# Performance work log

Hardware: AMD Instinct MI355X
Metric: run time of the kernel (lower is better)

## Reference

```python
import math
import jax, jax.numpy as jnp
import numpy as np

STEP = 0.1
EPS = 1e-12


def _laplacian(src, dst, n):
    # dense symmetric-normalized Laplacian from COO edge list (symmetrized, 0/1 weights)
    A = jnp.zeros((n, n), dtype=jnp.float32).at[src, dst].set(1.0)
    A = jnp.maximum(A, A.T)
    deg = A.sum(axis=1)
    dinv = jnp.where(deg > 0, 1.0 / jnp.sqrt(jnp.maximum(deg, 1e-12)), 0.0)
    return jnp.eye(n, dtype=jnp.float32) - dinv[:, None] * A * dinv[None, :]


def _filter_bank(L, bs):
    # rational band-pass bank centered at b in arange(0,2.1,STEP):
    # D_b = sqrt(2)*a * inv((L - b I)^4 + a I),  a = (STEP/2)^4
    n = L.shape[0]
    a = (STEP / 2.0) ** 4
    I = jnp.eye(n, dtype=L.dtype)

    def one(b):
        M1 = L - b * I
        P2 = M1 @ M1
        P4 = P2 @ P2
        return math.sqrt(2.0) * a * jnp.linalg.inv(P4 + a * I)

    return jax.vmap(one)(bs)  # [F, n, n]


def _cdist_mean(e):
    # mean pairwise euclidean distance, safe sqrt on the zero diagonal
    d2 = jnp.sum((e[:, None, :] - e[None, :, :]) ** 2, axis=-1)
    d = jnp.sqrt(jnp.where(d2 > 0, d2, 1.0))
    return jnp.where(d2 > 0, d, 0.0).mean()


def setup_inputs() -> dict:
    key = jax.random.key(0)
    k1, k2, k3, k4, k5 = jax.random.split(key, 5)
    B, N, F0, R, E = 64, 128, 32, 1118, 512
    return {
        "x": jax.random.normal(k1, (B, N, F0), dtype=jnp.float32),
        "random_signal": jax.random.normal(k2, (B, N, R), dtype=jnp.float32),
        "C": jax.random.normal(k3, (21, 1), dtype=jnp.float32),
        "edge_src": jax.random.randint(k4, (B, E), 0, N),
        "edge_dst": jax.random.randint(k5, (B, E), 0, N),
        "num_classes": 4,
    }


def reference(x, random_signal, C, edge_src, edge_dst, num_classes):
    B, N, _ = x.shape
    R = random_signal.shape[-1]
    # torch.normal(0, sqrt(1/R)) random signal concatenated to features
    feats = jnp.concatenate([x, random_signal * math.sqrt(1.0 / R)], axis=-1)  # [B,N,F0+R]
    bs = jnp.arange(0.0, 2.1, STEP, dtype=jnp.float32)  # [21]
    Cn = C / jnp.maximum(jnp.linalg.norm(C, axis=0, keepdims=True), EPS)  # F.normalize(C, dim=0)

    def per_graph(src, dst, xg):
        L = _laplacian(src, dst, N)
        D = _filter_bank(L, bs)                      # [F,N,N]
        L_hat = jnp.einsum('fnm,f->nm', D, Cn[:, 0])  # D.permute(1,2,0) @ C, squeezed
        A_hat = jnp.eye(N, dtype=xg.dtype) - L_hat
        y = A_hat @ xg                                # [N, F0+R]
        z = y / jnp.maximum(jnp.linalg.norm(y, axis=1, keepdims=True), EPS)
        logits = z @ z.T                              # decode_all on normalized x
        sp = -jnp.abs(logits).sum() / (N * N)         # -||logits||_1 / n^2
        return y.mean(axis=0), sp

    emb, sp_terms = jax.vmap(per_graph)(edge_src, edge_dst, feats)  # [B,D], [B]

    # faithful repeated in-loop division: s_{i+1} = (s_i + t_i)/B  =>  sum_i t_i * B^{-(B-i)}
    i = jnp.arange(B, dtype=jnp.float32)
    w = jnp.exp(-(B - i) * jnp.log(float(B)))
    sparsity_fwd = jnp.sum(sp_terms * w)

    # labels y = arange(B) % num_classes; one positive group (class members) and
    # one negative group (non-members) per class
    idx = np.arange(B)
    hl1 = jnp.float32(0.0)
    hl2 = jnp.float32(0.0)
    for c in range(num_classes):
        pos = jnp.asarray(idx[idx % num_classes == c])
        neg = jnp.asarray(idx[idx % num_classes != c])
        beta = 1.0 / num_classes + 1e-13  # one group per class
        hl1 = hl1 + (-_cdist_mean(emb[neg])) / beta
        hl2 = hl2 + _cdist_mean(emb[pos])

    Fk = C.shape[0]
    dims = jnp.sqrt(jnp.float32(Fk))
    c_l1 = jnp.sum(jnp.abs(C), axis=0)
    c_l2 = jnp.maximum(jnp.linalg.norm(C, axis=0), EPS)
    sparsity_c = jnp.mean((dims - c_l1 / c_l2) / (dims - 1.0))

    return sparsity_c + hl2 + hl1 + sparsity_fwd
```

## Files before the change

### kernel.cpp

```cpp
#include <hip/hip_runtime.h>
#include <math.h>

#define NN 128
#define SM 129
#define TS 132
#define RS 132
#define SS 17
#define SD 130
#define EP 132

typedef double d4 __attribute__((ext_vector_type(4)));

__global__ __launch_bounds__(256) void k1_lap(
    const int* __restrict__ src, const int* __restrict__ dst,
    int E, float* __restrict__ Lout) {
  extern __shared__ float sm1[];
  float* A    = sm1;
  float* dinv = sm1 + NN * SM;
  const int g   = blockIdx.x;
  const int tid = threadIdx.x;

  for (int e = tid; e < NN * NN; e += 256) {
    int i = e >> 7, j = e & 127;
    A[i * SM + j] = 0.f;
  }
  __syncthreads();
  const int* s = src + (size_t)g * E;
  const int* d = dst + (size_t)g * E;
  for (int e = tid; e < E; e += 256) {
    int a = s[e], b = d[e];
    A[a * SM + b] = 1.f;
    A[b * SM + a] = 1.f;
  }
  __syncthreads();
  if (tid < NN) {
    float acc = 0.f;
    for (int j = 0; j < NN; ++j) acc += A[tid * SM + j];
    dinv[tid] = (acc > 0.f) ? (float)(1.0 / sqrt((double)acc)) : 0.f;
  }
  __syncthreads();
  float* Lg = Lout + (size_t)g * NN * NN;
  for (int e = tid; e < NN * NN; e += 256) {
    int i = e >> 7, j = e & 127;
    Lg[e] = ((i == j) ? 1.f : 0.f) - dinv[i] * dinv[j] * A[i * SM + j];
  }
}

__global__ __launch_bounds__(512, 1) void kpow2(
    const float* __restrict__ L, double* __restrict__ L2) {
  extern __shared__ double Bs[];
  const int bid = blockIdx.x;
  const int g = bid >> 2, q = bid & 3;
  const int tid = threadIdx.x;
  const int wv = tid >> 6, ln = tid & 63;
  const int m  = ln & 15, kq = ln >> 4;
  const int rb = 32 * q + 16 * (wv & 1);
  const int cb0 = 2 * (wv >> 1);

  int rIdx[4], cIdx[4];
  {
    d4 z = {0.0, 0.0, 0.0, 0.0};
    d4 pr = __builtin_amdgcn_mfma_f64_16x16x4f64((double)m, 1.0, z, 0, 0, 0);
    d4 pc = __builtin_amdgcn_mfma_f64_16x16x4f64(1.0, (double)m, z, 0, 0, 0);
#pragma unroll
    for (int r = 0; r < 4; ++r) {
      rIdx[r] = ((int)(pr[r] * 0.25 + 0.5)) & 15;
      cIdx[r] = ((int)(pc[r] * 0.25 + 0.5)) & 15;
    }
  }

  const float* Lg = L + (size_t)g * NN * NN;
  for (int e = tid; e < NN * NN; e += 512) {
    int i = e >> 7, j = e & 127;
    Bs[i * SD + j] = (double)Lg[e];
  }
  __syncthreads();

  d4 acc[2];
#pragma unroll
  for (int c = 0; c < 2; ++c) {
    acc[c][0] = 0.0; acc[c][1] = 0.0; acc[c][2] = 0.0; acc[c][3] = 0.0;
  }
  for (int kc = 0; kc < 32; ++kc) {
    double a = Bs[(rb + m) * SD + 4 * kc + kq];
#pragma unroll
    for (int c = 0; c < 2; ++c) {
      double b = Bs[(4 * kc + kq) * SD + 16 * (cb0 + c) + m];
      acc[c] = __builtin_amdgcn_mfma_f64_16x16x4f64(a, b, acc[c], 0, 0, 0);
    }
  }
  double* out = L2 + (size_t)g * NN * NN;
#pragma unroll
  for (int c = 0; c < 2; ++c)
#pragma unroll
    for (int r = 0; r < 4; ++r)
      out[(rb + rIdx[r]) * NN + 16 * (cb0 + c) + cIdx[r]] = acc[c][r];
}

__global__ __launch_bounds__(512, 1) void kpow34(
    const float* __restrict__ L, const double* __restrict__ L2,
    double* __restrict__ L3, double* __restrict__ L4) {
  extern __shared__ double Bs[];
  const int bid = blockIdx.x;
  const int g = bid >> 2, h = (bid >> 1) & 1, job = bid & 1;
  const int tid = threadIdx.x;
  const int wv = tid >> 6, ln = tid & 63;
  const int m  = ln & 15, kq = ln >> 4;
  const int rb = 64 * h + 16 * (wv & 3);
  const int cb0 = 4 * (wv >> 2);

  int rIdx[4], cIdx[4];
  {
    d4 z = {0.0, 0.0, 0.0, 0.0};
    d4 pr = __builtin_amdgcn_mfma_f64_16x16x4f64((double)m, 1.0, z, 0, 0, 0);
    d4 pc = __builtin_amdgcn_mfma_f64_16x16x4f64(1.0, (double)m, z, 0, 0, 0);
#pragma unroll
    for (int r = 0; r < 4; ++r) {
      rIdx[r] = ((int)(pr[r] * 0.25 + 0.5)) & 15;
      cIdx[r] = ((int)(pc[r] * 0.25 + 0.5)) & 15;
    }
  }

  const float*  Lg  = L  + (size_t)g * NN * NN;
  const double* L2g = L2 + (size_t)g * NN * NN;
  if (job == 0) {
    for (int e = tid; e < NN * NN; e += 512) {
      int i = e >> 7, j = e & 127;
      Bs[i * SD + j] = (double)Lg[e];
    }
  } else {
    for (int e = tid; e < NN * NN; e += 512) {
      int i = e >> 7, j = e & 127;
      Bs[i * SD + j] = L2g[e];
    }
  }
  __syncthreads();

  d4 acc[4];
#pragma unroll
  for (int c = 0; c < 4; ++c) {
    acc[c][0] = 0.0; acc[c][1] = 0.0; acc[c][2] = 0.0; acc[c][3] = 0.0;
  }
  for (int kc = 0; kc < 32; ++kc) {
    double a = L2g[(rb + m) * NN + 4 * kc + kq];
#pragma unroll
    for (int c = 0; c < 4; ++c) {
      double b = Bs[(4 * kc + kq) * SD + 16 * (cb0 + c) + m];
      acc[c] = __builtin_amdgcn_mfma_f64_16x16x4f64(a, b, acc[c], 0, 0, 0);
    }
  }
  double* out = (job == 0 ? L3 : L4) + (size_t)g * NN * NN;
#pragma unroll
  for (int c = 0; c < 4; ++c)
#pragma unroll
    for (int r = 0; r < 4; ++r)
      out[(rb + rIdx[r]) * NN + 16 * (cb0 + c) + cIdx[r]] = acc[c][r];
}

__global__ __launch_bounds__(512, 4) void k2_filter(
    const float* __restrict__ L, const double* __restrict__ L2,
    const double* __restrict__ L3, const double* __restrict__ L4,
    const float* __restrict__ C, int NF, float* __restrict__ W) {
  extern __shared__ char smraw[];
  double* Rp  = (double*)smraw;
  double* Scd = (double*)(smraw + 16 * RS * 8);
  double* Pv  = (double*)(smraw + 16 * RS * 8 + 8 * 16 * SS * 8);

  const int bid = blockIdx.x;
  const int g = bid / NF, f = bid % NF;
  const int tid = threadIdx.x;
  const int wv = tid >> 6, ln = tid & 63;
  const int m  = ln & 15, kq = ln >> 4;
  double* S = Scd + wv * 16 * SS;

  double csum = 0.0;
  for (int q = 0; q < NF; ++q) { double c = (double)C[q]; csum += c * c; }
  double cn = sqrt(csum); if (cn < 1e-12) cn = 1e-12;
  const double a4 = 6.25e-6;
  const double coef = 1.4142135623730951 * a4 * ((double)C[f] / cn);
  const float  bf = (float)((double)f * 0.1);
  const double bb = (double)bf;
  const double c3 = -4.0 * bb;
  const double c2 = 6.0 * bb * bb;
  const double c1 = -4.0 * bb * bb * bb;
  const double c0 = bb * bb * bb * bb + a4;

  int rIdx[4], cIdx[4];
  {
    d4 z = {0.0, 0.0, 0.0, 0.0};
    d4 pr = __builtin_amdgcn_mfma_f64_16x16x4f64((double)m, 1.0, z, 0, 0, 0);
    d4 pc = __builtin_amdgcn_mfma_f64_16x16x4f64(1.0, (double)m, z, 0, 0, 0);
#pragma unroll
    for (int r = 0; r < 4; ++r) {
      rIdx[r] = ((int)(pr[r] * 0.25 + 0.5)) & 15;
      cIdx[r] = ((int)(pc[r] * 0.25 + 0.5)) & 15;
    }
  }

  const float*  Lg  = L  + (size_t)g * NN * NN;
  const double* L2g = L2 + (size_t)g * NN * NN;
  const double* L3g = L3 + (size_t)g * NN * NN;
  const double* L4g = L4 + (size_t)g * NN * NN;
  d4 T[8];
#pragma unroll
  for (int cb = 0; cb < 8; ++cb)
#pragma unroll
    for (int r = 0; r < 4; ++r) {
      int i = 16 * wv + rIdx[r], j = 16 * cb + cIdx[r];
      int idx = i * NN + j;
      double v = L4g[idx];
      v = fma(c3, L3g[idx], v);
      v = fma(c2, L2g[idx], v);
      v = fma(c1, (double)Lg[idx], v);
      if (i == j) v += c0;
      T[cb][r] = v;
    }

#pragma unroll 1
  for (int t = 0; t < 8; ++t) {
    if (wv == t) {
#pragma unroll
      for (int cb = 0; cb < 8; ++cb)
#pragma unroll
        for (int r = 0; r < 4; ++r)
          Rp[rIdx[r] * RS + 16 * cb + cIdx[r]] = T[cb][r];
    }
    __syncthreads();

    if (wv == t) {
      double sr[4];
#pragma unroll
      for (int r = 0; r < 4; ++r) sr[r] = Rp[(4 * r + kq) * RS + 16 * t + m];
#pragma unroll
      for (int k = 0; k < 16; ++k) {
        const int kr = k >> 2, kl = k & 3;
        double pv   = __shfl(sr[kr], 16 * kl + k);
        double rowv = __shfl(sr[kr], 16 * kl + m);
        double cv[4];
#pragma unroll
        for (int r = 0; r < 4; ++r) cv[r] = __shfl(sr[r], 16 * kq + k);
        double dp = 1.0 / pv;
#pragma unroll
        for (int r = 0; r < 4; ++r) {
          int i = 4 * r + kq;
          double nv;
          if (i == k)      nv = (m == k) ? dp : rowv * dp;
          else if (m == k) nv = -cv[r] * dp;
          else             nv = fma(-(cv[r] * dp), rowv, sr[r]);
          sr[r] = nv;
        }
      }
#pragma unroll
      for (int r = 0; r < 4; ++r) Pv[(4 * r + kq) * SS + m] = sr[r];
    }
    __syncthreads();

#pragma unroll
    for (int cb = 0; cb < 8; ++cb) {
      if (cb != t) continue;
      if (wv == t) {
#pragma unroll
        for (int r = 0; r < 4; ++r) T[cb][r] = Pv[rIdx[r] * SS + cIdx[r]];
      } else {
#pragma unroll
        for (int r = 0; r < 4; ++r) S[rIdx[r] * SS + cIdx[r]] = T[cb][r];
        __builtin_amdgcn_wave_barrier();
        d4 ncv = {0.0, 0.0, 0.0, 0.0};
#pragma unroll
        for (int kc = 0; kc < 4; ++kc) {
          double a = S[m * SS + 4 * kc + kq];
          double b = -Pv[(4 * kc + kq) * SS + m];
          ncv = __builtin_amdgcn_mfma_f64_16x16x4f64(a, b, ncv, 0, 0, 0);
        }
        T[cb] = ncv;
        __builtin_amdgcn_wave_barrier();
#pragma unroll
        for (int r = 0; r < 4; ++r) S[rIdx[r] * SS + cIdx[r]] = T[cb][r];
      }
    }
    __builtin_amdgcn_wave_barrier();

    const double* asrc = (wv == t) ? Pv : S;
#pragma unroll
    for (int cb = 0; cb < 8; ++cb) {
      if (cb == t) continue;
      d4 acc;
      if (wv == t) { acc[0] = 0.0; acc[1] = 0.0; acc[2] = 0.0; acc[3] = 0.0; }
      else         { acc = T[cb]; }
#pragma unroll
      for (int kc = 0; kc < 4; ++kc) {
        double a = asrc[m * SS + 4 * kc + kq];
        double b = Rp[(4 * kc + kq) * RS + 16 * cb + m];
        acc = __builtin_amdgcn_mfma_f64_16x16x4f64(a, b, acc, 0, 0, 0);
      }
      T[cb] = acc;
    }
    __syncthreads();
  }

  float* Wg = W + (size_t)g * NN * NN;
#pragma unroll
  for (int cb = 0; cb < 8; ++cb)
#pragma unroll
    for (int r = 0; r < 4; ++r)
      atomicAdd(&Wg[(16 * wv + rIdx[r]) * NN + 16 * cb + cIdx[r]],
                (float)(coef * T[cb][r]));
}

__global__ __launch_bounds__(512, 1) void k3_fused(
    const float* __restrict__ x, const float* __restrict__ rs,
    const float* __restrict__ W, float* __restrict__ G,
    float* __restrict__ emb, int F0, int R, int DTOT, int NCH,
    float rscale) {
  extern __shared__ float sm3[];
  float* ldsW = sm3;
  float* ldsX = sm3 + NN * TS;
  const int bid = blockIdx.x;
  const int g = bid / NCH;
  const int c = bid % NCH;
  const int d0 = c * 128;
  const int tid = threadIdx.x, tr = tid >> 4, tc = tid & 15;

  const float* Wg = W + (size_t)g * NN * NN;
  for (int e = tid; e < NN * NN; e += 512) {
    int k = e >> 7, i = e & 127;
    ldsW[k * TS + i] = Wg[e];
  }
  const float* xg = x + (size_t)g * NN * F0;
  const float* rg = rs + (size_t)g * NN * R;
  for (int e = tid; e < NN * NN; e += 512) {
    int k = e >> 7, dl = e & 127;
    int d = d0 + dl;
    float v = 0.f;
    if (d < DTOT) v = (d < F0) ? xg[k * F0 + d] : rg[k * R + (d - F0)] * rscale;
    ldsX[k * TS + dl] = v;
  }
  __syncthreads();

  float acc[4][8];
#pragma unroll
  for (int v = 0; v < 4; ++v)
#pragma unroll
    for (int u = 0; u < 8; ++u) acc[v][u] = 0.f;
  for (int k = 0; k < NN; ++k) {
    float4 w4 = *(const float4*)(ldsW + k * TS + 4 * tr);
    float xv[8];
#pragma unroll
    for (int u = 0; u < 8; ++u) xv[u] = ldsX[k * TS + tc + 16 * u];
    float wvv[4] = {w4.x, w4.y, w4.z, w4.w};
#pragma unroll
    for (int v = 0; v < 4; ++v)
#pragma unroll
      for (int u = 0; u < 8; ++u) acc[v][u] = fmaf(wvv[v], xv[u], acc[v][u]);
  }
#pragma unroll
  for (int v = 0; v < 4; ++v)
#pragma unroll
    for (int u = 0; u < 8; ++u)
      acc[v][u] = ldsX[(4 * tr + v) * TS + tc + 16 * u] - acc[v][u];
  __syncthreads();

#pragma unroll
  for (int v = 0; v < 4; ++v)
#pragma unroll
    for (int u = 0; u < 8; ++u)
      ldsW[(tc + 16 * u) * TS + 4 * tr + v] = acc[v][u];
#pragma unroll
  for (int u = 0; u < 8; ++u) {
    float s = 0.f;
#pragma unroll
    for (int v = 0; v < 4; ++v) s += acc[v][u];
    ldsX[tr * EP + tc + 16 * u] = s;
  }
  __syncthreads();

  float gg[4][8];
#pragma unroll
  for (int v = 0; v < 4; ++v)
#pragma unroll
    for (int u = 0; u < 8; ++u) gg[v][u] = 0.f;
  for (int dl = 0; dl < NN; ++dl) {
    float4 a4v = *(const float4*)(ldsW + dl * TS + 4 * tr);
    float bv[8];
#pragma unroll
    for (int u = 0; u < 8; ++u) bv[u] = ldsW[dl * TS + tc + 16 * u];
    float av[4] = {a4v.x, a4v.y, a4v.z, a4v.w};
#pragma unroll
    for (int v = 0; v < 4; ++v)
#pragma unroll
      for (int u = 0; u < 8; ++u) gg[v][u] = fmaf(av[v], bv[u], gg[v][u]);
  }
  float* Gg = G + (size_t)g * NN * NN;
#pragma unroll
  for (int v = 0; v < 4; ++v)
#pragma unroll
    for (int u = 0; u < 8; ++u)
      atomicAdd(&Gg[(4 * tr + v) * NN + tc + 16 * u], gg[v][u]);

  if (tid < 128) {
    int d = d0 + tid;
    if (d < DTOT) {
      float s = 0.f;
      for (int tt = 0; tt < 32; ++tt) s += ldsX[tt * EP + tid];
      emb[(size_t)g * 1152 + d] = s * (1.f / 128.f);
    }
  }
}

__global__ __launch_bounds__(256) void k45_fused(
    const float* __restrict__ G, double* __restrict__ spt,
    const float* __restrict__ emb, float* __restrict__ Dm, int DTOT) {
  __shared__ float inr[NN];
  __shared__ double red[4];
  const int bid = blockIdx.x, tid = threadIdx.x;
  if (bid < 64) {
    const int g = bid;
    const float* Gg = G + (size_t)g * NN * NN;
    if (tid < NN) {
      float n = sqrtf(fmaxf(Gg[tid * NN + tid], 0.f));
      inr[tid] = 1.f / fmaxf(n, 1e-12f);
    }
    __syncthreads();
    double s = 0.0;
    for (int e = tid; e < NN * NN; e += 256) {
      int i = e >> 7, j = e & 127;
      s += (double)(fabsf(Gg[e]) * inr[i] * inr[j]);
    }
    for (int off = 32; off; off >>= 1) s += __shfl_down(s, off);
    int wave = tid >> 6, lane = tid & 63;
    if (lane == 0) red[wave] = s;
    __syncthreads();
    if (tid == 0) spt[g] = -(red[0] + red[1] + red[2] + red[3]) / (double)(NN * NN);
  } else {
    const int i = bid - 64;
    const int wv = tid >> 6, l = tid & 63;
    float ei[18];
#pragma unroll
    for (int s = 0; s < 18; ++s) {
      int d = l + 64 * s;
      ei[s] = (d < DTOT) ? emb[(size_t)i * 1152 + d] : 0.f;
    }
    for (int jj = 0; jj < 16; ++jj) {
      int j = 4 * jj + wv;
      float acc = 0.f;
#pragma unroll
      for (int s = 0; s < 18; ++s) {
        int d = l + 64 * s;
        if (d < DTOT) {
          float df = ei[s] - emb[(size_t)j * 1152 + d];
          acc = fmaf(df, df, acc);
        }
      }
      for (int off = 32; off; off >>= 1) acc += __shfl_down(acc, off);
      if (l == 0) Dm[i * 64 + j] = (acc > 0.f) ? sqrtf(acc) : 0.f;
    }
  }
}

__global__ __launch_bounds__(64) void k5b_final(
    const float* __restrict__ Dm, const double* __restrict__ spt,
    const float* __restrict__ C, int NF,
    const int* __restrict__ ncls, float* __restrict__ out) {
  const int lane = threadIdx.x;
  const int nc = ncls[0];
  double spf = spt[lane] * exp(-((double)(64 - lane)) * log(64.0));
  for (int off = 32; off; off >>= 1) spf += __shfl_down(spf, off);

  double hl1 = 0.0, hl2 = 0.0;
  const double beta = 1.0 / (double)nc + 1e-13;
  for (int cc = 0; cc < nc; ++cc) {
    bool ip = (lane % nc) == cc;
    double ps = 0.0, ns = 0.0;
    for (int j = 0; j < 64; ++j) {
      double dv = (double)Dm[lane * 64 + j];
      bool jp = (j % nc) == cc;
      if (ip && jp) ps += dv;
      if (!ip && !jp) ns += dv;
    }
    for (int off = 32; off; off >>= 1) {
      ps += __shfl_down(ps, off);
      ns += __shfl_down(ns, off);
    }
    int npos = 0;
    for (int q = 0; q < 64; ++q) if (q % nc == cc) npos++;
    int nneg = 64 - npos;
    hl2 += ps / ((double)npos * (double)npos);
    hl1 += -(ns / ((double)nneg * (double)nneg)) / beta;
  }
  if (lane == 0) {
    double l1 = 0.0, l2 = 0.0;
    for (int q = 0; q < NF; ++q) { double cv = (double)C[q]; l1 += fabs(cv); l2 += cv * cv; }
    l2 = sqrt(l2); if (l2 < 1e-12) l2 = 1e-12;
    double dims = sqrt((double)NF);
    double sc = (dims - l1 / l2) / (dims - 1.0);
    out[0] = (float)(sc + hl2 + hl1 + spf);
  }
}

extern "C" void kernel_launch(void* const* d_in, const int* in_sizes, int n_in,
                              void* d_out, int out_size, void* d_ws, size_t ws_size,
                              hipStream_t stream) {
  (void)n_in; (void)out_size; (void)ws_size;
  const float* x    = (const float*)d_in[0];
  const float* rs   = (const float*)d_in[1];
  const float* C    = (const float*)d_in[2];
  const int*   esrc = (const int*)d_in[3];
  const int*   edst = (const int*)d_in[4];
  const int*   ncls = (const int*)d_in[5];
  float* out = (float*)d_out;

  const int F0   = in_sizes[0] / (64 * 128);
  const int R    = in_sizes[1] / (64 * 128);
  const int NF   = in_sizes[2];
  const int E    = in_sizes[3] / 64;
  const int DTOT = F0 + R;
  const int NCH  = (DTOT + 127) / 128;
  const float rscale = (float)(1.0 / sqrt((double)R));

  char* ws = (char*)d_ws;
  size_t off = 0;
  float*  L    = (float*)(ws + off);  off += (size_t)64 * NN * NN * 4;
  float*  W    = (float*)(ws + off);  off += (size_t)64 * NN * NN * 4;
  float*  G    = (float*)(ws + off);  off += (size_t)64 * NN * NN * 4;
  double* L2d  = (double*)(ws + off); off += (size_t)64 * NN * NN * 8;
  double* L3d  = (double*)(ws + off); off += (size_t)64 * NN * NN * 8;
  double* L4d  = (double*)(ws + off); off += (size_t)64 * NN * NN * 8;
  float*  emb  = (float*)(ws + off);  off += (size_t)64 * 1152 * 4;
  double* spt  = (double*)(ws + off); off += (size_t)64 * 8;
  float*  Dm   = (float*)(ws + off);  off += (size_t)64 * 64 * 4;

  hipMemsetAsync(W, 0, (size_t)2 * 64 * NN * NN * 4, stream);

  const int lds1 = (NN * SM + NN) * 4;
  const int ldsp = NN * SD * 8;
  const int lds2 = 16 * RS * 8 + 8 * 16 * SS * 8 + 16 * SS * 8;
  const int lds3 = NN * TS * 4 * 2;
  hipFuncSetAttribute((const void*)k1_lap,    hipFuncAttributeMaxDynamicSharedMemorySize, lds1);
  hipFuncSetAttribute((const void*)kpow2,     hipFuncAttributeMaxDynamicSharedMemorySize, ldsp);
  hipFuncSetAttribute((const void*)kpow34,    hipFuncAttributeMaxDynamicSharedMemorySize, ldsp);
  hipFuncSetAttribute((const void*)k2_filter, hipFuncAttributeMaxDynamicSharedMemorySize, lds2);
  hipFuncSetAttribute((const void*)k3_fused,  hipFuncAttributeMaxDynamicSharedMemorySize, lds3);

  k1_lap<<<64, 256, lds1, stream>>>(esrc, edst, E, L);
  kpow2<<<256, 512, ldsp, stream>>>(L, L2d);
  kpow34<<<256, 512, ldsp, stream>>>(L, L2d, L3d, L4d);
  k2_filter<<<64 * NF, 512, lds2, stream>>>(L, L2d, L3d, L4d, C, NF, W);
  k3_fused<<<64 * NCH, 512, lds3, stream>>>(x, rs, W, G, emb, F0, R, DTOT, NCH, rscale);
  k45_fused<<<128, 256, 0, stream>>>(G, spt, emb, Dm, DTOT);
  k5b_final<<<1, 64, 0, stream>>>(Dm, spt, C, NF, ncls, out);
}
```

Baseline: 637.1 us.

## Pipeline block Gauss-Jordan pivot inversion with double-buffered row panels

Restructures the blocked Gauss-Jordan inverse in the filter kernel so that, after each step's trailing update, the next pivot wave publishes its row panel and inverts its 16x16 pivot block immediately, writing into double-buffered LDS (Rp0/Rp1, Pv0/Pv1). This removes two of the three __syncthreads per step and lets the serial pivot inversion overlap with other waves' MFMA updates. It costs extra LDS per block, which may reduce occupancy, and adds more intra-wave barriers.

```diff
diff --git a/kernel.cpp b/kernel.cpp
--- a/kernel.cpp
+++ b/kernel.cpp
@@ -157,14 +157,38 @@
       out[(rb + rIdx[r]) * NN + 16 * (cb0 + c) + cIdx[r]] = acc[c][r];
 }
 
+__device__ __forceinline__ void gj16(double sr[4], int m, int kq) {
+#pragma unroll
+  for (int k = 0; k < 16; ++k) {
+    const int kr = k >> 2, kl = k & 3;
+    double pv   = __shfl(sr[kr], 16 * kl + k);
+    double rowv = __shfl(sr[kr], 16 * kl + m);
+    double cv[4];
+#pragma unroll
+    for (int r = 0; r < 4; ++r) cv[r] = __shfl(sr[r], 16 * kq + k);
+    double dp = 1.0 / pv;
+#pragma unroll
+    for (int r = 0; r < 4; ++r) {
+      int i = 4 * r + kq;
+      double nv;
+      if (i == k)      nv = (m == k) ? dp : rowv * dp;
+      else if (m == k) nv = -cv[r] * dp;
+      else             nv = fma(-(cv[r] * dp), rowv, sr[r]);
+      sr[r] = nv;
+    }
+  }
+}
+
 __global__ __launch_bounds__(512, 4) void k2_filter(
     const float* __restrict__ L, const double* __restrict__ L2,
     const double* __restrict__ L3, const double* __restrict__ L4,
     const float* __restrict__ C, int NF, float* __restrict__ W) {
   extern __shared__ char smraw[];
-  double* Rp  = (double*)smraw;
-  double* Scd = (double*)(smraw + 16 * RS * 8);
-  double* Pv  = (double*)(smraw + 16 * RS * 8 + 8 * 16 * SS * 8);
+  double* Rp0 = (double*)smraw;
+  double* Rp1 = Rp0 + 16 * RS;
+  double* Scd = Rp1 + 16 * RS;
+  double* Pv0 = Scd + 8 * 16 * SS;
+  double* Pv1 = Pv0 + 16 * SS;
 
   const int bid = blockIdx.x;
   const int g = bid / NF, f = bid % NF;
@@ -216,71 +240,53 @@
       T[cb][r] = v;
     }
 
+  if (wv == 0) {
+#pragma unroll
+    for (int cb = 0; cb < 8; ++cb)
+#pragma unroll
+      for (int r = 0; r < 4; ++r)
+        Rp0[rIdx[r] * RS + 16 * cb + cIdx[r]] = T[cb][r];
+#pragma unroll
+    for (int r = 0; r < 4; ++r) S[rIdx[r] * SS + cIdx[r]] = T[0][r];
+    __builtin_amdgcn_wave_barrier();
+    double sr[4];
+#pragma unroll
+    for (int r = 0; r < 4; ++r) sr[r] = S[(4 * r + kq) * SS + m];
+    gj16(sr, m, kq);
+#pragma unroll
+    for (int r = 0; r < 4; ++r) Pv0[(4 * r + kq) * SS + m] = sr[r];
+  }
+  __syncthreads();
+
 #pragma unroll 1
   for (int t = 0; t < 8; ++t) {
+    double* Rc = (t & 1) ? Rp1 : Rp0;
+    double* Rn = (t & 1) ? Rp0 : Rp1;
+    double* Pc = (t & 1) ? Pv1 : Pv0;
+    double* Pn = (t & 1) ? Pv0 : Pv1;
+
     if (wv == t) {
 #pragma unroll
-      for (int cb = 0; cb < 8; ++cb)
-#pragma unroll
-        for (int r = 0; r < 4; ++r)
-          Rp[rIdx[r] * RS + 16 * cb + cIdx[r]] = T[cb][r];
-    }
-    __syncthreads();
-
-    if (wv == t) {
-      double sr[4];
-#pragma unroll
-      for (int r = 0; r < 4; ++r) sr[r] = Rp[(4 * r + kq) * RS + 16 * t + m];
-#pragma unroll
-      for (int k = 0; k < 16; ++k) {
-        const int kr = k >> 2, kl = k & 3;
-        double pv   = __shfl(sr[kr], 16 * kl + k);
-        double rowv = __shfl(sr[kr], 16 * kl + m);
-        double cv[4];
-#pragma unroll
-        for (int r = 0; r < 4; ++r) cv[r] = __shfl(sr[r], 16 * kq + k);
-        double dp = 1.0 / pv;
-#pragma unroll
-        for (int r = 0; r < 4; ++r) {
-          int i = 4 * r + kq;
-          double nv;
-          if (i == k)      nv = (m == k) ? dp : rowv * dp;
-          else if (m == k) nv = -cv[r] * dp;
-          else             nv = fma(-(cv[r] * dp), rowv, sr[r]);
-          sr[r] = nv;
-        }
+      for (int r = 0; r < 4; ++r) T[t][r] = Pc[rIdx[r] * SS + cIdx[r]];
+    } else {
+#pragma unroll
+      for (int r = 0; r < 4; ++r) S[rIdx[r] * SS + cIdx[r]] = T[t][r];
+      __builtin_amdgcn_wave_barrier();
+      d4 ncv = {0.0, 0.0, 0.0, 0.0};
+#pragma unroll
+      for (int kc = 0; kc < 4; ++kc) {
+        double a = S[m * SS + 4 * kc + kq];
+        double b = -Pc[(4 * kc + kq) * SS + m];
+        ncv = __builtin_amdgcn_mfma_f64_16x16x4f64(a, b, ncv, 0, 0, 0);
       }
-#pragma unroll
-      for (int r = 0; r < 4; ++r) Pv[(4 * r + kq) * SS + m] = sr[r];
-    }
-    __syncthreads();
-
-#pragma unroll
-    for (int cb = 0; cb < 8; ++cb) {
-      if (cb != t) continue;
-      if (wv == t) {
-#pragma unroll
-        for (int r = 0; r < 4; ++r) T[cb][r] = Pv[rIdx[r] * SS + cIdx[r]];
-      } else {
-#pragma unroll
-        for (int r = 0; r < 4; ++r) S[rIdx[r] * SS + cIdx[r]] = T[cb][r];
-        __builtin_amdgcn_wave_barrier();
-        d4 ncv = {0.0, 0.0, 0.0, 0.0};
-#pragma unroll
-        for (int kc = 0; kc < 4; ++kc) {
-          double a = S[m * SS + 4 * kc + kq];
-          double b = -Pv[(4 * kc + kq) * SS + m];
-          ncv = __builtin_amdgcn_mfma_f64_16x16x4f64(a, b, ncv, 0, 0, 0);
-        }
-        T[cb] = ncv;
-        __builtin_amdgcn_wave_barrier();
-#pragma unroll
-        for (int r = 0; r < 4; ++r) S[rIdx[r] * SS + cIdx[r]] = T[cb][r];
-      }
-    }
-    __builtin_amdgcn_wave_barrier();
-
-    const double* asrc = (wv == t) ? Pv : S;
+      T[t] = ncv;
+      __builtin_amdgcn_wave_barrier();
+#pragma unroll
+      for (int r = 0; r < 4; ++r) S[rIdx[r] * SS + cIdx[r]] = T[t][r];
+      __builtin_amdgcn_wave_barrier();
+    }
+
+    const double* asrc = (wv == t) ? Pc : S;
 #pragma unroll
     for (int cb = 0; cb < 8; ++cb) {
       if (cb == t) continue;
@@ -290,10 +296,28 @@
 #pragma unroll
       for (int kc = 0; kc < 4; ++kc) {
         double a = asrc[m * SS + 4 * kc + kq];
-        double b = Rp[(4 * kc + kq) * RS + 16 * cb + m];
+        double b = Rc[(4 * kc + kq) * RS + 16 * cb + m];
         acc = __builtin_amdgcn_mfma_f64_16x16x4f64(a, b, acc, 0, 0, 0);
       }
       T[cb] = acc;
+    }
+
+    if (t < 7 && wv == t + 1) {
+      __builtin_amdgcn_wave_barrier();
+#pragma unroll
+      for (int cb = 0; cb < 8; ++cb)
+#pragma unroll
+        for (int r = 0; r < 4; ++r)
+          Rn[rIdx[r] * RS + 16 * cb + cIdx[r]] = T[cb][r];
+#pragma unroll
+      for (int r = 0; r < 4; ++r) S[rIdx[r] * SS + cIdx[r]] = T[t + 1][r];
+      __builtin_amdgcn_wave_barrier();
+      double sr[4];
+#pragma unroll
+      for (int r = 0; r < 4; ++r) sr[r] = S[(4 * r + kq) * SS + m];
+      gj16(sr, m, kq);
+#pragma unroll
+      for (int r = 0; r < 4; ++r) Pn[(4 * r + kq) * SS + m] = sr[r];
     }
     __syncthreads();
   }
@@ -533,7 +557,7 @@
 
   const int lds1 = (NN * SM + NN) * 4;
   const int ldsp = NN * SD * 8;
-  const int lds2 = 16 * RS * 8 + 8 * 16 * SS * 8 + 16 * SS * 8;
+  const int lds2 = 2 * 16 * RS * 8 + 8 * 16 * SS * 8 + 2 * 16 * SS * 8;
   const int lds3 = NN * TS * 4 * 2;
   hipFuncSetAttribute((const void*)k1_lap,    hipFuncAttributeMaxDynamicSharedMemorySize, lds1);
   hipFuncSetAttribute((const void*)kpow2,     hipFuncAttributeMaxDynamicSharedMemorySize, ldsp);
```

Result: slower. 935.4 us (+46.8%).

## Halve k3 shared memory by streaming W from global and aliasing the buffer

Applied to the files above, without the earlier changes.

The k3_fused kernel no longer stages the 128x128 W matrix in shared memory. Each thread now reads its float4 of W straight from global memory, with a one-step register prefetch, and the transposed result reuses the X buffer. The per-column embedding sums are now accumulated with LDS atomics into a small array. Together these cut LDS use from two tiles to one and raise launch_bounds to 4 blocks per CU, aiming for higher occupancy. The cost is a global load of W on every k iteration (likely cache hits) and contended LDS atomics.

```diff
diff --git a/kernel.cpp b/kernel.cpp
--- a/kernel.cpp
+++ b/kernel.cpp
@@ -307,25 +307,20 @@
                 (float)(coef * T[cb][r]));
 }
 
-__global__ __launch_bounds__(512, 1) void k3_fused(
+__global__ __launch_bounds__(512, 4) void k3_fused(
     const float* __restrict__ x, const float* __restrict__ rs,
     const float* __restrict__ W, float* __restrict__ G,
     float* __restrict__ emb, int F0, int R, int DTOT, int NCH,
     float rscale) {
   extern __shared__ float sm3[];
-  float* ldsW = sm3;
-  float* ldsX = sm3 + NN * TS;
+  float* ldsX = sm3;
+  float* embA = sm3 + NN * TS;
   const int bid = blockIdx.x;
   const int g = bid / NCH;
   const int c = bid % NCH;
   const int d0 = c * 128;
   const int tid = threadIdx.x, tr = tid >> 4, tc = tid & 15;
 
-  const float* Wg = W + (size_t)g * NN * NN;
-  for (int e = tid; e < NN * NN; e += 512) {
-    int k = e >> 7, i = e & 127;
-    ldsW[k * TS + i] = Wg[e];
-  }
   const float* xg = x + (size_t)g * NN * F0;
   const float* rg = rs + (size_t)g * NN * R;
   for (int e = tid; e < NN * NN; e += 512) {
@@ -335,15 +330,19 @@
     if (d < DTOT) v = (d < F0) ? xg[k * F0 + d] : rg[k * R + (d - F0)] * rscale;
     ldsX[k * TS + dl] = v;
   }
-  __syncthreads();
-
+  if (tid < NN) embA[tid] = 0.f;
+  __syncthreads();
+
+  const float* Wg = W + (size_t)g * NN * NN;
   float acc[4][8];
 #pragma unroll
   for (int v = 0; v < 4; ++v)
 #pragma unroll
     for (int u = 0; u < 8; ++u) acc[v][u] = 0.f;
+  float4 w4 = *(const float4*)(Wg + 4 * tr);
   for (int k = 0; k < NN; ++k) {
-    float4 w4 = *(const float4*)(ldsW + k * TS + 4 * tr);
+    float4 w4n;
+    if (k < NN - 1) w4n = *(const float4*)(Wg + (k + 1) * NN + 4 * tr);
     float xv[8];
 #pragma unroll
     for (int u = 0; u < 8; ++u) xv[u] = ldsX[k * TS + tc + 16 * u];
@@ -352,27 +351,32 @@
     for (int v = 0; v < 4; ++v)
 #pragma unroll
       for (int u = 0; u < 8; ++u) acc[v][u] = fmaf(wvv[v], xv[u], acc[v][u]);
+    w4 = w4n;
   }
 #pragma unroll
   for (int v = 0; v < 4; ++v)
 #pragma unroll
     for (int u = 0; u < 8; ++u)
       acc[v][u] = ldsX[(4 * tr + v) * TS + tc + 16 * u] - acc[v][u];
+
+#pragma unroll
+  for (int u = 0; u < 8; ++u) {
+    float s = acc[0][u] + acc[1][u] + acc[2][u] + acc[3][u];
+    atomicAdd(&embA[tc + 16 * u], s);
+  }
   __syncthreads();
 
 #pragma unroll
   for (int v = 0; v < 4; ++v)
 #pragma unroll
     for (int u = 0; u < 8; ++u)
-      ldsW[(tc + 16 * u) * TS + 4 * tr + v] = acc[v][u];
-#pragma unroll
-  for (int u = 0; u < 8; ++u) {
-    float s = 0.f;
-#pragma unroll
-    for (int v = 0; v < 4; ++v) s += acc[v][u];
-    ldsX[tr * EP + tc + 16 * u] = s;
-  }
-  __syncthreads();
+      ldsX[(tc + 16 * u) * TS + 4 * tr + v] = acc[v][u];
+  __syncthreads();
+
+  if (tid < 128) {
+    int d = d0 + tid;
+    if (d < DTOT) emb[(size_t)g * 1152 + d] = embA[tid] * (1.f / 128.f);
+  }
 
   float gg[4][8];
 #pragma unroll
@@ -380,10 +384,10 @@
 #pragma unroll
     for (int u = 0; u < 8; ++u) gg[v][u] = 0.f;
   for (int dl = 0; dl < NN; ++dl) {
-    float4 a4v = *(const float4*)(ldsW + dl * TS + 4 * tr);
+    float4 a4v = *(const float4*)(ldsX + dl * TS + 4 * tr);
     float bv[8];
 #pragma unroll
-    for (int u = 0; u < 8; ++u) bv[u] = ldsW[dl * TS + tc + 16 * u];
+    for (int u = 0; u < 8; ++u) bv[u] = ldsX[dl * TS + tc + 16 * u];
     float av[4] = {a4v.x, a4v.y, a4v.z, a4v.w};
 #pragma unroll
     for (int v = 0; v < 4; ++v)
@@ -396,15 +400,6 @@
 #pragma unroll
     for (int u = 0; u < 8; ++u)
       atomicAdd(&Gg[(4 * tr + v) * NN + tc + 16 * u], gg[v][u]);
-
-  if (tid < 128) {
-    int d = d0 + tid;
-    if (d < DTOT) {
-      float s = 0.f;
-      for (int tt = 0; tt < 32; ++tt) s += ldsX[tt * EP + tid];
-      emb[(size_t)g * 1152 + d] = s * (1.f / 128.f);
-    }
-  }
 }
 
 __global__ __launch_bounds__(256) void k45_fused(
@@ -534,7 +529,7 @@
   const int lds1 = (NN * SM + NN) * 4;
   const int ldsp = NN * SD * 8;
   const int lds2 = 16 * RS * 8 + 8 * 16 * SS * 8 + 16 * SS * 8;
-  const int lds3 = NN * TS * 4 * 2;
+  const int lds3 = (NN * TS + NN) * 4;
   hipFuncSetAttribute((const void*)k1_lap,    hipFuncAttributeMaxDynamicSharedMemorySize, lds1);
   hipFuncSetAttribute((const void*)kpow2,     hipFuncAttributeMaxDynamicSharedMemorySize, ldsp);
   hipFuncSetAttribute((const void*)kpow34,    hipFuncAttributeMaxDynamicSharedMemorySize, ldsp);
```

Result: faster. 601.8 us (-5.6%).
